# Kernel optimization log

Measured on AMD Instinct MI355X. Metric: run time of the kernel, lower is better.

The kernel has to match this reference:

```python
import jax, jax.numpy as jnp
import numpy as np

HEADS = 8
HEAD_DIM = 64
DIM = HEADS * HEAD_DIM  # 512
K = 7  # kernel_size (square)


def setup_inputs() -> dict:
    key = jax.random.key(0)
    ks = jax.random.split(key, 5)
    B, H, W = 1, 80, 80
    x = jax.random.normal(ks[0], (B, H, W, DIM), jnp.float32)
    qkv_w = jax.random.normal(ks[1], (3 * DIM, DIM), jnp.float32) * 0.02
    qkv_b = jnp.zeros((3 * DIM,), jnp.float32)
    rpb = jax.random.normal(ks[2], (HEADS, 2 * K - 1, 2 * K - 1), jnp.float32) * 0.02
    proj_w = jax.random.normal(ks[3], (DIM, DIM), jnp.float32) * 0.02
    proj_b = jnp.zeros((DIM,), jnp.float32)
    return {"x": x, "qkv_w": qkv_w, "qkv_b": qkv_b, "rpb": rpb,
            "proj_w": proj_w, "proj_b": proj_b}


def _window_indices(L, k):
    # NATTEN-style clamped neighborhood: window of size k fully in-bounds,
    # centered at the query when possible.
    starts = jnp.clip(jnp.arange(L) - k // 2, 0, L - k)          # [L]
    idx = starts[:, None] + jnp.arange(k)[None, :]               # [L, k] neighbor coords
    off = idx - jnp.arange(L)[:, None] + (k - 1)                 # [L, k] rpb index in [0, 2k-2]
    return idx, off


def reference(x, qkv_w, qkv_b, rpb, proj_w, proj_b):
    B, H, W, C = x.shape
    n, hd, k = HEADS, HEAD_DIM, K

    qkv = (x @ qkv_w.T + qkv_b).reshape(B, H, W, 3, n, hd)
    qkv = qkv.transpose(3, 0, 4, 1, 2, 5)                        # [3,B,n,H,W,hd]
    q, kk, v = qkv[0], qkv[1], qkv[2]
    q = q * (hd ** -0.5)

    idx_h, off_h = _window_indices(H, k)                         # [H,k]
    idx_w, off_w = _window_indices(W, k)                         # [W,k]

    # Gather neighborhood windows: [B,n,H,k,W,k,hd]
    k_nb = kk[:, :, idx_h][:, :, :, :, idx_w]
    v_nb = v[:, :, idx_h][:, :, :, :, idx_w]

    # attn logits: q[b,n,i,j,d] . k_nb[b,n,i,a,j,c,d] -> [B,n,H,W,k,k]
    attn = jnp.einsum('bnijd,bniajcd->bnijac', q, k_nb)

    # relative position bias: rpb[h, off_h[i,a], off_w[j,c]] -> [n,H,k,W,k]
    bias = rpb[:, off_h[:, :, None, None], off_w[None, None, :, :]]
    attn = attn + bias.transpose(0, 1, 3, 2, 4)[None]            # -> [1,n,H,W,k,k]

    a = jax.nn.softmax(attn.reshape(B, n, H, W, k * k), axis=-1)
    a = a.reshape(B, n, H, W, k, k)

    out = jnp.einsum('bnijac,bniajcd->bnijd', a, v_nb)           # [B,n,H,W,hd]
    out = out.transpose(0, 2, 3, 1, 4).reshape(B, H, W, C)
    out = out @ proj_w.T + proj_b
    return out
```

## Files before the change

### kernel.cpp

```cpp
#include <hip/hip_runtime.h>
#include <hip/hip_bf16.h>


typedef __attribute__((ext_vector_type(4))) float f32x4;
typedef __attribute__((ext_vector_type(8))) short bf16x8;
typedef __attribute__((ext_vector_type(4))) short s16x4;

#define HEADS 8
#define HEAD_DIM 64
#define DIM 512
#define KW 7
#define HH 80
#define WW 80
#define NPIX (HH * WW)

__device__ inline unsigned short f2bf(float f) {
    union { __hip_bfloat16 b; unsigned short u; } cvt;
    cvt.b = __float2bfloat16(f);
    return cvt.u;
}
__device__ inline float bf2f(short s) {
    union { float f; unsigned u; } c;
    c.u = ((unsigned)(unsigned short)s) << 16;
    return c.f;
}

__device__ inline void storeC(float* p, float v) { *p = v; }
__device__ inline void storeC(__hip_bfloat16* p, float v) { *p = __float2bfloat16(v); }

__device__ inline void g2l16(const void* g, void* l) {
    __builtin_amdgcn_global_load_lds(
        (const __attribute__((address_space(1))) unsigned int*)g,
        (__attribute__((address_space(3))) unsigned int*)l,
        16, 0, 0);
}

__global__ __launch_bounds__(256) void cast3_f32_bf16(
    const float* __restrict__ a, short* __restrict__ oa, int na4,
    const float* __restrict__ b, short* __restrict__ ob, int nb4,
    const float* __restrict__ c, short* __restrict__ oc, int nc4)
{
    int i = blockIdx.x * 256 + threadIdx.x;
    const float* src; short* dst; int idx;
    if (i < na4) { src = a; dst = oa; idx = i; }
    else if (i < na4 + nb4) { src = b; dst = ob; idx = i - na4; }
    else if (i < na4 + nb4 + nc4) { src = c; dst = oc; idx = i - na4 - nb4; }
    else return;
    f32x4 v = reinterpret_cast<const f32x4*>(src)[idx];
    s16x4 r;
#pragma unroll
    for (int j = 0; j < 4; ++j) r[j] = (short)f2bf(v[j]);
    reinterpret_cast<s16x4*>(dst)[idx] = r;
}

template <typename CT>
__global__ __launch_bounds__(256) void gemm_lds(
    const __hip_bfloat16* __restrict__ A,
    const __hip_bfloat16* __restrict__ W,
    const float* __restrict__ bias,
    CT* __restrict__ C,
    int M, int N, int K)
{
    __shared__ short lds[2][2][128][64];

    const int lane = threadIdx.x & 63;
    const int wv = threadIdx.x >> 6;
    const int wr = wv >> 1;
    const int wc = wv & 1;
    const int r0 = blockIdx.y * 128;
    const int c0 = blockIdx.x * 128;
    const int rf = lane & 15;
    const int kg = lane >> 4;

    const int NT = K >> 6;

    auto stage = [&](const __hip_bfloat16* src, int rowbase, int kb, short* dst) {
#pragma unroll
        for (int q = 0; q < 4; ++q) {
            const int L = wv * 256 + q * 64 + lane;
            const int r = L >> 3;
            const int cs = (L & 7) ^ (r & 7);
            g2l16(src + (size_t)(rowbase + r) * K + kb + cs * 8, dst + (size_t)L * 8);
        }
    };
    auto frag = [&](const short* base, int row, int ch) -> bf16x8 {
        return *reinterpret_cast<const bf16x8*>(base + row * 64 + ((ch ^ (row & 7)) << 3));
    };

    f32x4 acc[4][4] = {};

    stage(A, r0, 0, &lds[0][0][0][0]);
    stage(W, c0, 0, &lds[0][1][0][0]);
    __syncthreads();

    int cur = 0;
    for (int t = 0; t < NT; ++t) {
        if (t + 1 < NT) {
            stage(A, r0, (t + 1) * 64, &lds[cur ^ 1][0][0][0]);
            stage(W, c0, (t + 1) * 64, &lds[cur ^ 1][1][0][0]);
        }
        const short* la = &lds[cur][0][0][0];
        const short* lb = &lds[cur][1][0][0];
#pragma unroll
        for (int ks = 0; ks < 2; ++ks) {
            bf16x8 af[4], bfr[4];
#pragma unroll
            for (int i = 0; i < 4; ++i)
                af[i] = frag(la, wr * 64 + i * 16 + rf, ks * 4 + kg);
#pragma unroll
            for (int j = 0; j < 4; ++j)
                bfr[j] = frag(lb, wc * 64 + j * 16 + rf, ks * 4 + kg);
#pragma unroll
            for (int i = 0; i < 4; ++i)
#pragma unroll
                for (int j = 0; j < 4; ++j)
                    acc[i][j] = __builtin_amdgcn_mfma_f32_16x16x32_bf16(af[i], bfr[j], acc[i][j], 0, 0, 0);
        }
        __syncthreads();
        cur ^= 1;
    }

#pragma unroll
    for (int j = 0; j < 4; ++j) {
        const int col = c0 + wc * 64 + j * 16 + rf;
        const float bcol = bias[col];
#pragma unroll
        for (int i = 0; i < 4; ++i) {
#pragma unroll
            for (int r = 0; r < 4; ++r) {
                const int row = r0 + wr * 64 + i * 16 + kg * 4 + r;
                storeC(C + (size_t)row * N + col, acc[i][j][r] + bcol);
            }
        }
    }
}

__global__ __launch_bounds__(256) void natten_tiled(
    const __hip_bfloat16* __restrict__ qkv,
    const float* __restrict__ rpb,
    __hip_bfloat16* __restrict__ aout)
{
    __shared__ short sK[196][72];
    __shared__ short sV[196][72];
    __shared__ float sW[64][52];
    __shared__ float sB[169];

    const int tid = threadIdx.x;
    const int h = blockIdx.y;
    const int ti = blockIdx.x / 10;
    const int tj = blockIdx.x - ti * 10;
    const int R0 = ti * 8 - 3;
    const int C0 = tj * 8 - 3;

    if (tid < 169) sB[tid] = rpb[h * 169 + tid];

#pragma unroll
    for (int it = 0; it < 7; ++it) {
        const int task = it * 256 + tid;
        if (task < 1568) {
            const int slot = task >> 3;
            const int ch = task & 7;
            const int r = slot / 14;
            const int c = slot - r * 14;
            int gi = R0 + r; gi = gi < 0 ? 0 : (gi > 79 ? 79 : gi);
            int gj = C0 + c; gj = gj < 0 ? 0 : (gj > 79 ? 79 : gj);
            const __hip_bfloat16* src =
                qkv + ((size_t)(gi * WW + gj) * 1536 + 512 + h * 64 + ch * 8);
            bf16x8 kv = *reinterpret_cast<const bf16x8*>(src);
            bf16x8 vv = *reinterpret_cast<const bf16x8*>(src + 512);
            *reinterpret_cast<bf16x8*>(&sK[slot][ch * 8]) = kv;
            *reinterpret_cast<bf16x8*>(&sV[slot][ch * 8]) = vv;
        }
    }
    __syncthreads();

    const int lane = tid & 63;
    const int wv = tid >> 6;
    const int p = wv * 16 + (lane >> 2);
    const int g = lane & 3;
    const int pi_l = p >> 3, pj_l = p & 7;
    const int pi = ti * 8 + pi_l, pj = tj * 8 + pj_l;
    int si = pi - 3; si = si < 0 ? 0 : (si > (HH - KW) ? (HH - KW) : si);
    int sj = pj - 3; sj = sj < 0 ? 0 : (sj > (WW - KW) ? (WW - KW) : sj);
    const int si_l = si - R0;
    const int sj_l = sj - C0;
    const int oh = si - pi + 6;
    const int ow = sj - pj + 6;

    float qf[16];
    {
        const __hip_bfloat16* qsrc =
            qkv + ((size_t)(pi * WW + pj) * 1536 + h * 64 + g * 16);
        bf16x8 q0 = *reinterpret_cast<const bf16x8*>(qsrc);
        bf16x8 q1 = *reinterpret_cast<const bf16x8*>(qsrc + 8);
#pragma unroll
        for (int j = 0; j < 8; ++j) {
            qf[j] = 0.125f * bf2f(q0[j]);
            qf[8 + j] = 0.125f * bf2f(q1[j]);
        }
    }

    for (int a = 0; a < KW; ++a) {
        const int rbase = (si_l + a) * 14 + sj_l;
        const float* brow = &sB[(oh + a) * 13 + ow];
#pragma unroll
        for (int c = 0; c < KW; ++c) {
            const int slot = rbase + c;
            bf16x8 k0 = *reinterpret_cast<const bf16x8*>(&sK[slot][g * 16]);
            bf16x8 k1 = *reinterpret_cast<const bf16x8*>(&sK[slot][g * 16 + 8]);
            float d = 0.f;
#pragma unroll
            for (int j = 0; j < 8; ++j) d += qf[j] * bf2f(k0[j]);
#pragma unroll
            for (int j = 0; j < 8; ++j) d += qf[8 + j] * bf2f(k1[j]);
            d += __shfl_xor(d, 1, 64);
            d += __shfl_xor(d, 2, 64);
            if (g == 0) sW[p][a * KW + c] = d + brow[c];
        }
    }

    float m = -1e30f;
    for (int i = 0; i < 49; ++i) m = fmaxf(m, sW[p][i]);
    float s = 0.f;
    for (int i = 0; i < 49; ++i) {
        const float e = __expf(sW[p][i] - m);
        s += e;
        if (g == 0) sW[p][i] = e;
    }
    const float rs = 1.0f / s;

    float o[16];
#pragma unroll
    for (int j = 0; j < 16; ++j) o[j] = 0.f;
    for (int a = 0; a < KW; ++a) {
        const int rbase = (si_l + a) * 14 + sj_l;
#pragma unroll
        for (int c = 0; c < KW; ++c) {
            const int slot = rbase + c;
            const float w = sW[p][a * KW + c];
            bf16x8 v0 = *reinterpret_cast<const bf16x8*>(&sV[slot][g * 16]);
            bf16x8 v1 = *reinterpret_cast<const bf16x8*>(&sV[slot][g * 16 + 8]);
#pragma unroll
            for (int j = 0; j < 8; ++j) o[j] += w * bf2f(v0[j]);
#pragma unroll
            for (int j = 0; j < 8; ++j) o[8 + j] += w * bf2f(v1[j]);
        }
    }

    bf16x8 r0v, r1v;
#pragma unroll
    for (int j = 0; j < 8; ++j) {
        r0v[j] = (short)f2bf(o[j] * rs);
        r1v[j] = (short)f2bf(o[8 + j] * rs);
    }
    __hip_bfloat16* dst = aout + ((size_t)(pi * WW + pj) * 512 + h * 64 + g * 16);
    *reinterpret_cast<bf16x8*>(dst) = r0v;
    *reinterpret_cast<bf16x8*>(dst + 8) = r1v;
}

extern "C" void kernel_launch(void* const* d_in, const int* in_sizes, int n_in,
                              void* d_out, int out_size, void* d_ws, size_t ws_size,
                              hipStream_t stream) {
    const float* x      = (const float*)d_in[0];
    const float* qkv_w  = (const float*)d_in[1];
    const float* qkv_b  = (const float*)d_in[2];
    const float* rpb    = (const float*)d_in[3];
    const float* proj_w = (const float*)d_in[4];
    const float* proj_b = (const float*)d_in[5];
    float* out = (float*)d_out;

    char* wsb = (char*)d_ws;
    __hip_bfloat16* xb    = (__hip_bfloat16*)wsb;
    __hip_bfloat16* wqkv  = (__hip_bfloat16*)(wsb + 6553600);
    __hip_bfloat16* wproj = (__hip_bfloat16*)(wsb + 8126464);
    __hip_bfloat16* qkv   = (__hip_bfloat16*)(wsb + 8650752);
    __hip_bfloat16* aout  = (__hip_bfloat16*)(wsb + 28311552);

    dim3 blk(256);
    cast3_f32_bf16<<<dim3((819200 + 196608 + 65536 + 255) / 256), blk, 0, stream>>>(
        x, (short*)xb, 819200, qkv_w, (short*)wqkv, 196608, proj_w, (short*)wproj, 65536);

    gemm_lds<__hip_bfloat16><<<dim3((3 * DIM) / 128, NPIX / 128), blk, 0, stream>>>(
        xb, wqkv, qkv_b, qkv, NPIX, 3 * DIM, DIM);

    natten_tiled<<<dim3(100, 8), blk, 0, stream>>>(qkv, rpb, aout);

    gemm_lds<float><<<dim3(DIM / 128, NPIX / 128), blk, 0, stream>>>(
        aout, wproj, proj_b, out, NPIX, DIM, DIM);
}
```

Measured before the change: 149.3 us.

## Read K/V neighborhoods directly from global memory instead of staging in LDS

Drops the shared-memory staging of the 14x14 K/V halo tile and has each thread load its neighbor K/V vectors straight from global (relying on L1/L2 cache), while fully unrolling the window loops. It also splits the softmax max/sum across the four lanes of a pixel with shuffle reductions instead of each lane scanning all 49 values. This removes LDS footprint and a staging pass, which may raise occupancy, but it relies on caches to absorb the roughly 49x redundant global reads per pixel.

```diff
diff --git a/kernel.cpp b/kernel.cpp
--- a/kernel.cpp
+++ b/kernel.cpp
@@ -135,13 +135,11 @@
     }
 }
 
-__global__ __launch_bounds__(256) void natten_tiled(
+__global__ __launch_bounds__(256) void natten_direct(
     const __hip_bfloat16* __restrict__ qkv,
     const float* __restrict__ rpb,
     __hip_bfloat16* __restrict__ aout)
 {
-    __shared__ short sK[196][72];
-    __shared__ short sV[196][72];
     __shared__ float sW[64][52];
     __shared__ float sB[169];
 
@@ -149,48 +147,26 @@
     const int h = blockIdx.y;
     const int ti = blockIdx.x / 10;
     const int tj = blockIdx.x - ti * 10;
-    const int R0 = ti * 8 - 3;
-    const int C0 = tj * 8 - 3;
 
     if (tid < 169) sB[tid] = rpb[h * 169 + tid];
-
-#pragma unroll
-    for (int it = 0; it < 7; ++it) {
-        const int task = it * 256 + tid;
-        if (task < 1568) {
-            const int slot = task >> 3;
-            const int ch = task & 7;
-            const int r = slot / 14;
-            const int c = slot - r * 14;
-            int gi = R0 + r; gi = gi < 0 ? 0 : (gi > 79 ? 79 : gi);
-            int gj = C0 + c; gj = gj < 0 ? 0 : (gj > 79 ? 79 : gj);
-            const __hip_bfloat16* src =
-                qkv + ((size_t)(gi * WW + gj) * 1536 + 512 + h * 64 + ch * 8);
-            bf16x8 kv = *reinterpret_cast<const bf16x8*>(src);
-            bf16x8 vv = *reinterpret_cast<const bf16x8*>(src + 512);
-            *reinterpret_cast<bf16x8*>(&sK[slot][ch * 8]) = kv;
-            *reinterpret_cast<bf16x8*>(&sV[slot][ch * 8]) = vv;
-        }
-    }
     __syncthreads();
 
     const int lane = tid & 63;
     const int wv = tid >> 6;
     const int p = wv * 16 + (lane >> 2);
     const int g = lane & 3;
-    const int pi_l = p >> 3, pj_l = p & 7;
-    const int pi = ti * 8 + pi_l, pj = tj * 8 + pj_l;
+    const int pi = ti * 8 + (p >> 3);
+    const int pj = tj * 8 + (p & 7);
     int si = pi - 3; si = si < 0 ? 0 : (si > (HH - KW) ? (HH - KW) : si);
     int sj = pj - 3; sj = sj < 0 ? 0 : (sj > (WW - KW) ? (WW - KW) : sj);
-    const int si_l = si - R0;
-    const int sj_l = sj - C0;
     const int oh = si - pi + 6;
     const int ow = sj - pj + 6;
 
+    const __hip_bfloat16* qkv_hd = qkv + h * 64 + g * 16;
+
     float qf[16];
     {
-        const __hip_bfloat16* qsrc =
-            qkv + ((size_t)(pi * WW + pj) * 1536 + h * 64 + g * 16);
+        const __hip_bfloat16* qsrc = qkv_hd + (size_t)(pi * WW + pj) * 1536;
         bf16x8 q0 = *reinterpret_cast<const bf16x8*>(qsrc);
         bf16x8 q1 = *reinterpret_cast<const bf16x8*>(qsrc + 8);
 #pragma unroll
@@ -200,14 +176,15 @@
         }
     }
 
+#pragma unroll
     for (int a = 0; a < KW; ++a) {
-        const int rbase = (si_l + a) * 14 + sj_l;
+        const int rbase = (si + a) * WW + sj;
         const float* brow = &sB[(oh + a) * 13 + ow];
 #pragma unroll
         for (int c = 0; c < KW; ++c) {
-            const int slot = rbase + c;
-            bf16x8 k0 = *reinterpret_cast<const bf16x8*>(&sK[slot][g * 16]);
-            bf16x8 k1 = *reinterpret_cast<const bf16x8*>(&sK[slot][g * 16 + 8]);
+            const __hip_bfloat16* kp = qkv_hd + (size_t)(rbase + c) * 1536 + 512;
+            bf16x8 k0 = *reinterpret_cast<const bf16x8*>(kp);
+            bf16x8 k1 = *reinterpret_cast<const bf16x8*>(kp + 8);
             float d = 0.f;
 #pragma unroll
             for (int j = 0; j < 8; ++j) d += qf[j] * bf2f(k0[j]);
@@ -220,26 +197,31 @@
     }
 
     float m = -1e30f;
-    for (int i = 0; i < 49; ++i) m = fmaxf(m, sW[p][i]);
+    for (int i = g; i < 49; i += 4) m = fmaxf(m, sW[p][i]);
+    m = fmaxf(m, __shfl_xor(m, 1, 64));
+    m = fmaxf(m, __shfl_xor(m, 2, 64));
     float s = 0.f;
-    for (int i = 0; i < 49; ++i) {
+    for (int i = g; i < 49; i += 4) {
         const float e = __expf(sW[p][i] - m);
         s += e;
-        if (g == 0) sW[p][i] = e;
-    }
+        sW[p][i] = e;
+    }
+    s += __shfl_xor(s, 1, 64);
+    s += __shfl_xor(s, 2, 64);
     const float rs = 1.0f / s;
 
     float o[16];
 #pragma unroll
     for (int j = 0; j < 16; ++j) o[j] = 0.f;
+#pragma unroll
     for (int a = 0; a < KW; ++a) {
-        const int rbase = (si_l + a) * 14 + sj_l;
+        const int rbase = (si + a) * WW + sj;
 #pragma unroll
         for (int c = 0; c < KW; ++c) {
-            const int slot = rbase + c;
             const float w = sW[p][a * KW + c];
-            bf16x8 v0 = *reinterpret_cast<const bf16x8*>(&sV[slot][g * 16]);
-            bf16x8 v1 = *reinterpret_cast<const bf16x8*>(&sV[slot][g * 16 + 8]);
+            const __hip_bfloat16* vp = qkv_hd + (size_t)(rbase + c) * 1536 + 1024;
+            bf16x8 v0 = *reinterpret_cast<const bf16x8*>(vp);
+            bf16x8 v1 = *reinterpret_cast<const bf16x8*>(vp + 8);
 #pragma unroll
             for (int j = 0; j < 8; ++j) o[j] += w * bf2f(v0[j]);
 #pragma unroll
@@ -283,7 +265,7 @@
     gemm_lds<__hip_bfloat16><<<dim3((3 * DIM) / 128, NPIX / 128), blk, 0, stream>>>(
         xb, wqkv, qkv_b, qkv, NPIX, 3 * DIM, DIM);
 
-    natten_tiled<<<dim3(100, 8), blk, 0, stream>>>(qkv, rpb, aout);
+    natten_direct<<<dim3(100, 8), blk, 0, stream>>>(qkv, rpb, aout);
 
     gemm_lds<float><<<dim3(DIM / 128, NPIX / 128), blk, 0, stream>>>(
         aout, wproj, proj_b, out, NPIX, DIM, DIM);
```

Result: slower. 165.1 us (+10.6%).
